# Kernel optimization log

Hardware: AMD Instinct MI355X
Metric: run time of the kernel (lower is better)

Reference implementation:

```python
import jax, jax.numpy as jnp
import numpy as np

K = 10
A_JAC = 0.5
B_JAC = 0.5
N_NODES = 100000
N_EDGES = 1600000
IN_CH, HID, OUT_CH = 256, 64, 32
NUM_LAYERS = 2


def setup_inputs() -> dict:
    key = jax.random.key(0)
    k1, k2, k3, k4, k5, k6 = jax.random.split(key, 6)
    x = jax.random.normal(k1, (N_NODES, IN_CH), dtype=jnp.float32)
    edge_index = jax.random.randint(k2, (2, N_EDGES), 0, N_NODES, dtype=jnp.int64)
    W1 = jax.random.normal(k3, (IN_CH, HID), dtype=jnp.float32) / np.sqrt(IN_CH)
    b1 = jnp.zeros((HID,), dtype=jnp.float32)
    coeffs = jnp.ones((NUM_LAYERS, K + 1), dtype=jnp.float32) / (K + 1)
    W2 = jax.random.normal(k4, (HID, OUT_CH), dtype=jnp.float32) / np.sqrt(HID)
    b2 = jnp.zeros((OUT_CH,), dtype=jnp.float32)
    return {"x": x, "edge_index": edge_index, "W1": W1, "b1": b1,
            "coeffs": coeffs, "W2": W2, "b2": b2}


def _build_norm(edge_index, num_nodes):
    # add self loops (as PyG add_self_loops does)
    loops = jnp.arange(num_nodes, dtype=edge_index.dtype)
    row = jnp.concatenate([edge_index[0], loops])
    col = jnp.concatenate([edge_index[1], loops])
    deg = jax.ops.segment_sum(jnp.ones_like(col, dtype=jnp.float32), col,
                              num_segments=num_nodes)
    dinv = jnp.where(deg > 0, deg ** -0.5, 0.0)
    norm = dinv[row] * dinv[col]  # [E + N]
    return row, col, norm


def _propagate(h, row, col, norm, num_nodes):
    # out[i] = sum_{e: col[e]=i} norm[e] * h[row[e]]
    return jax.ops.segment_sum(norm[:, None] * h[row], col, num_segments=num_nodes)


def _jacobi_conv(h, row, col, norm, c, num_nodes):
    a, b = A_JAC, B_JAC
    Tx0 = h
    out = c[0] * Tx0
    Tx1 = _propagate(h, row, col, norm, num_nodes)
    out = out + c[1] * Tx1
    for k in range(2, K + 1):
        n = k - 1
        A_n = (2 * n + a + b + 1) * (2 * n + a + b + 2) / (2 * (n + 1) * (n + a + b + 1))
        B_n = (a ** 2 - b ** 2) * (2 * n + a + b + 1) / (2 * (n + 1) * (n + a + b + 1) * (2 * n + a + b))
        C_n = (n + a) * (n + b) * (2 * n + a + b + 2) / ((n + 1) * (n + a + b + 1) * (2 * n + a + b))
        Tx2 = A_n * _propagate(Tx1, row, col, norm, num_nodes) + B_n * Tx1 - C_n * Tx0
        out = out + c[k] * Tx2
        Tx0, Tx1 = Tx1, Tx2
    return out


def reference(x, edge_index, W1, b1, coeffs, W2, b2):
    num_nodes = x.shape[0]
    row, col, norm = _build_norm(edge_index, num_nodes)
    h = jax.nn.relu(x @ W1 + b1)
    for l in range(NUM_LAYERS):
        h = jax.nn.relu(_jacobi_conv(h, row, col, norm, coeffs[l], num_nodes))
    return h @ W2 + b2
```

## Files before the change

### kernel.cpp

```cpp
#include <hip/hip_runtime.h>
#include <hip/hip_fp16.h>

#define NN 100000
#define NE 1600000
#define KORD 10
#define HID 64
#define SCAN_BLK 1024
#define NBLK ((NN + SCAN_BLK - 1) / SCAN_BLK)

typedef _Float16 half8v __attribute__((ext_vector_type(8)));
typedef _Float16 half4v __attribute__((ext_vector_type(4)));
typedef float float4v __attribute__((ext_vector_type(4)));

__device__ __forceinline__ float2 up2(unsigned u) {
    __half2 hh = *(__half2*)&u;
    return __half22float2(hh);
}
__device__ __forceinline__ unsigned pk2(float a, float b) {
    __half2 hh = __floats2half2_rn(a, b);
    return *(unsigned*)&hh;
}

__global__ __launch_bounds__(256) void k_zero(int* __restrict__ cnt,
                                              int* __restrict__ dhist) {
    int i = blockIdx.x * 256 + threadIdx.x;
    if (i < NN) cnt[i] = 0;
    if (i < 64) dhist[i] = 0;
}

__global__ __launch_bounds__(256) void k_hist(const int* __restrict__ ei,
                                              int* __restrict__ cnt) {
    int e = blockIdx.x * 256 + threadIdx.x;
    if (e < NE) atomicAdd(&cnt[ei[NE + e]], 1);
}

__global__ __launch_bounds__(256) void k_dinv(const int* __restrict__ cnt,
                                              float* __restrict__ dinv) {
    int i = blockIdx.x * 256 + threadIdx.x;
    if (i < NN) dinv[i] = rsqrtf((float)(cnt[i] + 1));
}

__global__ __launch_bounds__(SCAN_BLK) void k_scan1(const int* __restrict__ cnt,
                                                    int* __restrict__ cursor,
                                                    int* __restrict__ bsum) {
    __shared__ int tmp[SCAN_BLK];
    int t = threadIdx.x;
    int g = blockIdx.x * SCAN_BLK + t;
    int v = (g < NN) ? cnt[g] : 0;
    tmp[t] = v;
    __syncthreads();
    int x = v;
    for (int off = 1; off < SCAN_BLK; off <<= 1) {
        int y = (t >= off) ? tmp[t - off] : 0;
        __syncthreads();
        x += y;
        tmp[t] = x;
        __syncthreads();
    }
    if (g < NN) cursor[g] = x - v;
    if (t == SCAN_BLK - 1) bsum[blockIdx.x] = x;
}

__global__ __launch_bounds__(128) void k_scan2(int* __restrict__ bsum) {
    __shared__ int tmp[128];
    int t = threadIdx.x;
    int v = (t < NBLK) ? bsum[t] : 0;
    tmp[t] = v;
    __syncthreads();
    int x = v;
    for (int off = 1; off < 128; off <<= 1) {
        int y = (t >= off) ? tmp[t - off] : 0;
        __syncthreads();
        x += y;
        tmp[t] = x;
        __syncthreads();
    }
    if (t < NBLK) bsum[t] = x - v;
}

__global__ __launch_bounds__(SCAN_BLK) void k_scan3(int* __restrict__ cursor,
                                                    const int* __restrict__ bsum,
                                                    int* __restrict__ ccur) {
    int g = blockIdx.x * SCAN_BLK + threadIdx.x;
    if (g < NN) {
        int v = cursor[g] + bsum[blockIdx.x];
        cursor[g] = v;
        ccur[g] = v;
    }
    if (g == 0) cursor[NN] = NE;
}

__global__ __launch_bounds__(256) void k_scatter(const int* __restrict__ ei,
                                                 int* __restrict__ ccur,
                                                 int* __restrict__ csr) {
    int e = blockIdx.x * 256 + threadIdx.x;
    if (e >= NE) return;
    int r = ei[e], c = ei[NE + e];
    int pos = atomicAdd(&ccur[c], 1);
    csr[pos] = r;
}

__global__ __launch_bounds__(256) void k_dhist(const int* __restrict__ cnt,
                                               int* __restrict__ dhist) {
    __shared__ int lh[64];
    int t = threadIdx.x;
    if (t < 64) lh[t] = 0;
    __syncthreads();
    int i = blockIdx.x * 256 + t;
    if (i < NN) atomicAdd(&lh[min(cnt[i], 63)], 1);
    __syncthreads();
    if (t < 64 && lh[t]) atomicAdd(&dhist[t], lh[t]);
}

__global__ void k_dscan(int* __restrict__ dhist) {
    __shared__ int tmp[64];
    int t = threadIdx.x;
    int v = dhist[t];
    tmp[t] = v;
    __syncthreads();
    int x = v;
    for (int off = 1; off < 64; off <<= 1) {
        int y = (t >= off) ? tmp[t - off] : 0;
        __syncthreads();
        x += y;
        tmp[t] = x;
        __syncthreads();
    }
    dhist[t] = x - v;
}

__global__ __launch_bounds__(256) void k_dperm(const int* __restrict__ cnt,
                                               int* __restrict__ dhist,
                                               int* __restrict__ perm) {
    __shared__ int lh[64], lb[64];
    int t = threadIdx.x;
    if (t < 64) lh[t] = 0;
    __syncthreads();
    int i = blockIdx.x * 256 + t;
    int b = 0, my = 0;
    if (i < NN) { b = min(cnt[i], 63); my = atomicAdd(&lh[b], 1); }
    __syncthreads();
    if (t < 64) lb[t] = lh[t] ? atomicAdd(&dhist[t], lh[t]) : 0;
    __syncthreads();
    if (i < NN) perm[lb[b] + my] = i;
}

__global__ __launch_bounds__(256) void k_zrow(__half* __restrict__ a, __half* __restrict__ b,
                                              __half* __restrict__ c, __half* __restrict__ d) {
    int t = threadIdx.x;
    __half z = __float2half(0.f);
    size_t base = (size_t)NN * HID;
    if (t < 64)       a[base + t] = z;
    else if (t < 128) b[base + (t - 64)] = z;
    else if (t < 192) c[base + (t - 128)] = z;
    else              d[base + (t - 192)] = z;
}

__global__ __launch_bounds__(256) void k_prepw1(const float* __restrict__ W1,
                                                _Float16* __restrict__ W1T) {
    int f = blockIdx.x * 256 + threadIdx.x;
    int n = f >> 8, k = f & 255;
    W1T[f] = (_Float16)W1[k * 64 + n];
}

#define G1K 128
#define G1S 136
__global__ __launch_bounds__(256) void k_gemm1(const float* __restrict__ x,
                                               const _Float16* __restrict__ W1T,
                                               const float* __restrict__ b1,
                                               const float* __restrict__ dinv,
                                               __half* __restrict__ h) {
    __shared__ _Float16 A_lds[64 * G1S];
    __shared__ _Float16 B_lds[64 * G1S];
    int t = threadIdx.x;
    int wave = t >> 6, lane = t & 63;
    int quad = lane >> 4, m16 = lane & 15;
    int row0 = blockIdx.x * 64;

    float4v acc[4];
#pragma unroll
    for (int n4 = 0; n4 < 4; ++n4) acc[n4] = (float4v){0.f, 0.f, 0.f, 0.f};

    for (int c = 0; c < 2; ++c) {
        int k0 = c * G1K;
#pragma unroll
        for (int i = 0; i < 8; ++i) {
            int f = i * 256 + t;
            int r = f >> 5, c4 = f & 31;
            int grow = row0 + r;
            float4 v = (grow < NN) ? *(const float4*)&x[(size_t)grow * 256 + k0 + c4 * 4]
                                   : make_float4(0.f, 0.f, 0.f, 0.f);
            half4v hv = {(_Float16)v.x, (_Float16)v.y, (_Float16)v.z, (_Float16)v.w};
            *(half4v*)&A_lds[r * G1S + c4 * 4] = hv;
        }
#pragma unroll
        for (int i = 0; i < 4; ++i) {
            int f = i * 256 + t;
            int n = f >> 4, k8 = f & 15;
            *(half8v*)&B_lds[n * G1S + k8 * 8] =
                *(const half8v*)&W1T[n * 256 + k0 + k8 * 8];
        }
        __syncthreads();

#pragma unroll
        for (int s = 0; s < 4; ++s) {
            half8v af = *(const half8v*)&A_lds[(wave * 16 + m16) * G1S + s * 32 + quad * 8];
#pragma unroll
            for (int n4 = 0; n4 < 4; ++n4) {
                half8v bf = *(const half8v*)&B_lds[(n4 * 16 + m16) * G1S + s * 32 + quad * 8];
                acc[n4] = __builtin_amdgcn_mfma_f32_16x16x32_f16(af, bf, acc[n4], 0, 0, 0);
            }
        }
        __syncthreads();
    }

    float bv[4];
#pragma unroll
    for (int n4 = 0; n4 < 4; ++n4) bv[n4] = b1[n4 * 16 + m16];
#pragma unroll
    for (int r = 0; r < 4; ++r) {
        int grow = row0 + wave * 16 + quad * 4 + r;
        if (grow >= NN) continue;
        float dv = dinv[grow];
#pragma unroll
        for (int n4 = 0; n4 < 4; ++n4) {
            float v = dv * fmaxf(acc[n4][r] + bv[n4], 0.f);
            h[(size_t)grow * 64 + n4 * 16 + m16] = __float2half(v);
        }
    }
}

__global__ __launch_bounds__(256) void k_prop(const int* __restrict__ cursor,
                                              const int* __restrict__ csr,
                                              const int* __restrict__ perm,
                                              const __half* __restrict__ src,
                                              const __half* __restrict__ t0,
                                              const float* __restrict__ dinv,
                                              __half* __restrict__ dst,
                                              __half* __restrict__ acc,
                                              __half* __restrict__ hout,
                                              float An, float Bn, float Cn,
                                              const float* __restrict__ coeffs,
                                              int cbase, int kidx, int init,
                                              int finalize, int unscale) {
    int slot = ((blockIdx.x * 256 + threadIdx.x) >> 6) * 8 + ((threadIdx.x & 63) >> 3);
    int ch8 = (threadIdx.x & 7) * 8;
    bool valid = slot < NN;
    int node = valid ? perm[slot] : 0;
    int beg = valid ? cursor[node] : 0;
    int end = valid ? cursor[node + 1] : 0;

    int len = end - beg;
    int q = len >> 2;
    int j0 = beg,          e0 = beg + q;
    int j1 = e0,           e1 = beg + 2 * q;
    int j2 = e1,           e2 = beg + 3 * q;
    int j3 = e2,           e3 = end;

    float p[8];
#pragma unroll
    for (int i = 0; i < 8; ++i) p[i] = 0.f;

    while (__any(j3 < e3)) {
        int a0 = (j0 < e0) ? j0 : 0;
        int a1 = (j1 < e1) ? j1 : 0;
        int a2 = (j2 < e2) ? j2 : 0;
        int a3 = (j3 < e3) ? j3 : 0;
        int v0 = csr[a0], v1 = csr[a1], v2 = csr[a2], v3 = csr[a3];
        int r0 = (j0 < e0) ? v0 : NN;
        int r1 = (j1 < e1) ? v1 : NN;
        int r2 = (j2 < e2) ? v2 : NN;
        int r3 = (j3 < e3) ? v3 : NN;
        uint4 u0 = *(const uint4*)&src[(size_t)r0 * HID + ch8];
        uint4 u1 = *(const uint4*)&src[(size_t)r1 * HID + ch8];
        uint4 u2 = *(const uint4*)&src[(size_t)r2 * HID + ch8];
        uint4 u3 = *(const uint4*)&src[(size_t)r3 * HID + ch8];
        {
            float2 f0 = up2(u0.x), f1 = up2(u0.y), f2 = up2(u0.z), f3 = up2(u0.w);
            p[0] += f0.x; p[1] += f0.y; p[2] += f1.x; p[3] += f1.y;
            p[4] += f2.x; p[5] += f2.y; p[6] += f3.x; p[7] += f3.y;
        }
        {
            float2 f0 = up2(u1.x), f1 = up2(u1.y), f2 = up2(u1.z), f3 = up2(u1.w);
            p[0] += f0.x; p[1] += f0.y; p[2] += f1.x; p[3] += f1.y;
            p[4] += f2.x; p[5] += f2.y; p[6] += f3.x; p[7] += f3.y;
        }
        {
            float2 f0 = up2(u2.x), f1 = up2(u2.y), f2 = up2(u2.z), f3 = up2(u2.w);
            p[0] += f0.x; p[1] += f0.y; p[2] += f1.x; p[3] += f1.y;
            p[4] += f2.x; p[5] += f2.y; p[6] += f3.x; p[7] += f3.y;
        }
        {
            float2 f0 = up2(u3.x), f1 = up2(u3.y), f2 = up2(u3.z), f3 = up2(u3.w);
            p[0] += f0.x; p[1] += f0.y; p[2] += f1.x; p[3] += f1.y;
            p[4] += f2.x; p[5] += f2.y; p[6] += f3.x; p[7] += f3.y;
        }
        ++j0; ++j1; ++j2; ++j3;
    }

    if (!valid) return;
    size_t idx = (size_t)node * HID + ch8;
    float dv = dinv[node];
    float dv2 = dv * dv;

    uint4 sr = *(const uint4*)&src[idx];
    float2 s01 = up2(sr.x), s23 = up2(sr.y), s45 = up2(sr.z), s67 = up2(sr.w);
    float sv[8] = {s01.x, s01.y, s23.x, s23.y, s45.x, s45.y, s67.x, s67.y};

    uint4 tr = *(const uint4*)&t0[idx];
    float2 t01 = up2(tr.x), t23 = up2(tr.y), t45 = up2(tr.z), t67 = up2(tr.w);
    float tv[8] = {t01.x, t01.y, t23.x, t23.y, t45.x, t45.y, t67.x, t67.y};

    float v[8];
#pragma unroll
    for (int i = 0; i < 8; ++i)
        v[i] = An * dv2 * (p[i] + sv[i]) + Bn * sv[i] - Cn * tv[i];

    if (!finalize) {
        uint4 o;
        o.x = pk2(v[0], v[1]); o.y = pk2(v[2], v[3]);
        o.z = pk2(v[4], v[5]); o.w = pk2(v[6], v[7]);
        *(uint4*)&dst[idx] = o;
    }

    float ck = coeffs[cbase + kidx];
    float av[8];
    if (init) {
        float c0 = coeffs[cbase];
#pragma unroll
        for (int i = 0; i < 8; ++i) av[i] = c0 * sv[i];
    } else {
        uint4 ar = *(const uint4*)&acc[idx];
        float2 a01 = up2(ar.x), a23 = up2(ar.y), a45 = up2(ar.z), a67 = up2(ar.w);
        av[0] = a01.x; av[1] = a01.y; av[2] = a23.x; av[3] = a23.y;
        av[4] = a45.x; av[5] = a45.y; av[6] = a67.x; av[7] = a67.y;
    }
#pragma unroll
    for (int i = 0; i < 8; ++i) av[i] += ck * v[i];

    uint4 o;
    if (finalize) {
        float s = unscale ? (1.0f / dv) : 1.0f;
        o.x = pk2(s * fmaxf(av[0], 0.f), s * fmaxf(av[1], 0.f));
        o.y = pk2(s * fmaxf(av[2], 0.f), s * fmaxf(av[3], 0.f));
        o.z = pk2(s * fmaxf(av[4], 0.f), s * fmaxf(av[5], 0.f));
        o.w = pk2(s * fmaxf(av[6], 0.f), s * fmaxf(av[7], 0.f));
        *(uint4*)&hout[idx] = o;
    } else {
        o.x = pk2(av[0], av[1]); o.y = pk2(av[2], av[3]);
        o.z = pk2(av[4], av[5]); o.w = pk2(av[6], av[7]);
        *(uint4*)&acc[idx] = o;
    }
}

__global__ __launch_bounds__(256) void k_gemm2(const __half* __restrict__ h,
                                               const float* __restrict__ W2,
                                               const float* __restrict__ b2,
                                               float* __restrict__ out) {
    __shared__ float W2s[64 * 32];
    __shared__ float b2s[32];
    int t = threadIdx.x;
    for (int i = t * 4; i < 64 * 32; i += 256 * 4)
        *(float4*)&W2s[i] = *(const float4*)&W2[i];
    if (t < 32) b2s[t] = b2[t];
    __syncthreads();

    int gid = blockIdx.x * 256 + t;
    int row = gid >> 3;
    int c4 = (t & 7) * 4;
    if (row >= NN) return;
    const __half* hr = h + (size_t)row * 64;
    float4 acc = *(const float4*)&b2s[c4];
#pragma unroll
    for (int k8 = 0; k8 < 8; ++k8) {
        uint4 raw = *(const uint4*)&hr[k8 * 8];
        float2 a01 = up2(raw.x), a23 = up2(raw.y), a45 = up2(raw.z), a67 = up2(raw.w);
        float a[8] = {a01.x, a01.y, a23.x, a23.y, a45.x, a45.y, a67.x, a67.y};
#pragma unroll
        for (int j = 0; j < 8; ++j) {
            float4 w = *(const float4*)&W2s[(k8 * 8 + j) * 32 + c4];
            acc.x += a[j] * w.x;
            acc.y += a[j] * w.y;
            acc.z += a[j] * w.z;
            acc.w += a[j] * w.w;
        }
    }
    *(float4*)&out[(size_t)row * 32 + c4] = acc;
}

extern "C" void kernel_launch(void* const* d_in, const int* in_sizes, int n_in,
                              void* d_out, int out_size, void* d_ws, size_t ws_size,
                              hipStream_t stream) {
    const float* x      = (const float*)d_in[0];
    const int*   ei     = (const int*)d_in[1];
    const float* W1     = (const float*)d_in[2];
    const float* b1     = (const float*)d_in[3];
    const float* coeffs = (const float*)d_in[4];
    const float* W2     = (const float*)d_in[5];
    const float* b2     = (const float*)d_in[6];
    float* out = (float*)d_out;

    char* ws = (char*)d_ws;
    size_t off = 0;
    auto alloc = [&](size_t bytes) { void* p = ws + off; off += (bytes + 255) & ~(size_t)255; return p; };
    int*      cnt    = (int*)alloc(NN * 4);
    int*      cursor = (int*)alloc((NN + 1) * 4);
    int*      ccur   = (int*)alloc(NN * 4);
    int*      bsum   = (int*)alloc(NBLK * 4);
    float*    dinv   = (float*)alloc(NN * 4);
    int*      csr    = (int*)alloc((size_t)NE * 4);
    int*      dhist  = (int*)alloc(64 * 4);
    int*      perm   = (int*)alloc(NN * 4);
    _Float16* W1T    = (_Float16*)alloc(256 * 64 * 2);
    __half*   h16    = (__half*)alloc((size_t)(NN + 1) * HID * 2);
    __half*   bufA   = (__half*)alloc((size_t)(NN + 1) * HID * 2);
    __half*   bufB   = (__half*)alloc((size_t)(NN + 1) * HID * 2);
    __half*   bufC   = (__half*)alloc((size_t)(NN + 1) * HID * 2);
    __half*   accb   = (__half*)alloc((size_t)NN * HID * 2);

    const int BN = (NN + 255) / 256;
    const int BE = (NE + 255) / 256;
    const int BP = (NN + 31) / 32;

    k_zero<<<BN, 256, 0, stream>>>(cnt, dhist);
    k_hist<<<BE, 256, 0, stream>>>(ei, cnt);
    k_dinv<<<BN, 256, 0, stream>>>(cnt, dinv);
    k_scan1<<<NBLK, SCAN_BLK, 0, stream>>>(cnt, cursor, bsum);
    k_scan2<<<1, 128, 0, stream>>>(bsum);
    k_scan3<<<NBLK, SCAN_BLK, 0, stream>>>(cursor, bsum, ccur);
    k_scatter<<<BE, 256, 0, stream>>>(ei, ccur, csr);

    k_dhist<<<BN, 256, 0, stream>>>(cnt, dhist);
    k_dscan<<<1, 64, 0, stream>>>(dhist);
    k_dperm<<<BN, 256, 0, stream>>>(cnt, dhist, perm);
    k_zrow<<<1, 256, 0, stream>>>(h16, bufA, bufB, bufC);

    k_prepw1<<<64, 256, 0, stream>>>(W1, W1T);
    k_gemm1<<<(NN + 63) / 64, 256, 0, stream>>>(x, W1T, b1, dinv, h16);

    __half* rot[4] = {h16, bufA, bufB, bufC};

    for (int l = 0; l < 2; ++l) {
        int cbase = l * (KORD + 1);
        k_prop<<<BP, 256, 0, stream>>>(cursor, csr, perm, rot[0], rot[0], dinv,
                                       rot[1], accb, h16, 1.0f, 0.0f, 0.0f,
                                       coeffs, cbase, 1, 1, 0, 0);
        for (int k = 2; k <= KORD; ++k) {
            __half* dst = rot[k & 3];
            const __half* s1 = rot[(k - 1) & 3];
            const __half* s0 = rot[(k - 2) & 3];
            double n = k - 1, a = 0.5, b = 0.5;
            double An = (2*n + a + b + 1) * (2*n + a + b + 2) / (2 * (n + 1) * (n + a + b + 1));
            double Bn = (a*a - b*b) * (2*n + a + b + 1) / (2 * (n + 1) * (n + a + b + 1) * (2*n + a + b));
            double Cn = (n + a) * (n + b) * (2*n + a + b + 2) / ((n + 1) * (n + a + b + 1) * (2*n + a + b));
            k_prop<<<BP, 256, 0, stream>>>(cursor, csr, perm, s1, s0, dinv,
                                           dst, accb, h16, (float)An, (float)Bn, (float)Cn,
                                           coeffs, cbase, k, 0,
                                           (k == KORD) ? 1 : 0, l);
        }
    }

    k_gemm2<<<(NN * 8 + 255) / 256, 256, 0, stream>>>(h16, W2, b2, out);
}
```

Before: 1.173 ms.

## Build CSR with two-pass bucketed binning instead of global atomic scatter

Replaces the histogram, three-kernel scan and atomic scatter CSR build with a two-level bucket sort. The first pass bins edges into 256-node buckets using shared-memory atomics and packs the local column and source row into one word. The second pass sorts each bucket in LDS and also writes the degree, dinv and cursor. This cuts global atomics and kernel launches, but adds a fixed per-bucket capacity (BCAP) that silently drops edges if a bucket overflows, and assumes the row index fits in 24 bits.

```diff
diff --git a/kernel.cpp b/kernel.cpp
--- a/kernel.cpp
+++ b/kernel.cpp
@@ -5,8 +5,10 @@
 #define NE 1600000
 #define KORD 10
 #define HID 64
-#define SCAN_BLK 1024
-#define NBLK ((NN + SCAN_BLK - 1) / SCAN_BLK)
+
+#define NBUK ((NN + 255) / 256)
+#define BCAP 8192
+#define EPB  (NE / 256)
 
 typedef _Float16 half8v __attribute__((ext_vector_type(8)));
 typedef _Float16 half4v __attribute__((ext_vector_type(4)));
@@ -21,83 +23,104 @@
     return *(unsigned*)&hh;
 }
 
-__global__ __launch_bounds__(256) void k_zero(int* __restrict__ cnt,
+__global__ __launch_bounds__(512) void k_zero(int* __restrict__ gcnt,
                                               int* __restrict__ dhist) {
-    int i = blockIdx.x * 256 + threadIdx.x;
-    if (i < NN) cnt[i] = 0;
-    if (i < 64) dhist[i] = 0;
-}
-
-__global__ __launch_bounds__(256) void k_hist(const int* __restrict__ ei,
-                                              int* __restrict__ cnt) {
-    int e = blockIdx.x * 256 + threadIdx.x;
-    if (e < NE) atomicAdd(&cnt[ei[NE + e]], 1);
-}
-
-__global__ __launch_bounds__(256) void k_dinv(const int* __restrict__ cnt,
-                                              float* __restrict__ dinv) {
-    int i = blockIdx.x * 256 + threadIdx.x;
-    if (i < NN) dinv[i] = rsqrtf((float)(cnt[i] + 1));
-}
-
-__global__ __launch_bounds__(SCAN_BLK) void k_scan1(const int* __restrict__ cnt,
-                                                    int* __restrict__ cursor,
-                                                    int* __restrict__ bsum) {
-    __shared__ int tmp[SCAN_BLK];
-    int t = threadIdx.x;
-    int g = blockIdx.x * SCAN_BLK + t;
-    int v = (g < NN) ? cnt[g] : 0;
+    int t = threadIdx.x;
+    if (t < NBUK) gcnt[t] = 0;
+    if (t < 64) dhist[t] = 0;
+}
+
+__global__ __launch_bounds__(1024) void k_binA(const int* __restrict__ ei,
+                                               int* __restrict__ gcnt,
+                                               unsigned* __restrict__ staged) {
+    __shared__ int lh[NBUK];
+    __shared__ int lcur[NBUK];
+    int t = threadIdx.x;
+    int ebeg = blockIdx.x * EPB;
+    int eend = min(ebeg + EPB, NE);
+    for (int i = t; i < NBUK; i += 1024) lh[i] = 0;
+    __syncthreads();
+    for (int e = ebeg + t; e < eend; e += 1024)
+        atomicAdd(&lh[ei[NE + e] >> 8], 1);
+    __syncthreads();
+    for (int i = t; i < NBUK; i += 1024)
+        lcur[i] = lh[i] ? atomicAdd(&gcnt[i], lh[i]) : 0;
+    __syncthreads();
+    for (int e = ebeg + t; e < eend; e += 1024) {
+        int r = ei[e], c = ei[NE + e];
+        int bkt = c >> 8;
+        int slot = atomicAdd(&lcur[bkt], 1);
+        if (slot < BCAP)
+            staged[(size_t)bkt * BCAP + slot] = ((unsigned)(c & 255) << 24) | (unsigned)r;
+    }
+}
+
+__global__ __launch_bounds__(512) void k_bscan(const int* __restrict__ gcnt,
+                                               int* __restrict__ bbase,
+                                               int* __restrict__ cursor) {
+    __shared__ int tmp[512];
+    int t = threadIdx.x;
+    int v = (t < NBUK) ? gcnt[t] : 0;
     tmp[t] = v;
     __syncthreads();
     int x = v;
-    for (int off = 1; off < SCAN_BLK; off <<= 1) {
+    for (int off = 1; off < 512; off <<= 1) {
         int y = (t >= off) ? tmp[t - off] : 0;
         __syncthreads();
         x += y;
         tmp[t] = x;
         __syncthreads();
     }
-    if (g < NN) cursor[g] = x - v;
-    if (t == SCAN_BLK - 1) bsum[blockIdx.x] = x;
-}
-
-__global__ __launch_bounds__(128) void k_scan2(int* __restrict__ bsum) {
-    __shared__ int tmp[128];
-    int t = threadIdx.x;
-    int v = (t < NBLK) ? bsum[t] : 0;
-    tmp[t] = v;
-    __syncthreads();
-    int x = v;
-    for (int off = 1; off < 128; off <<= 1) {
-        int y = (t >= off) ? tmp[t - off] : 0;
-        __syncthreads();
-        x += y;
-        tmp[t] = x;
-        __syncthreads();
-    }
-    if (t < NBLK) bsum[t] = x - v;
-}
-
-__global__ __launch_bounds__(SCAN_BLK) void k_scan3(int* __restrict__ cursor,
-                                                    const int* __restrict__ bsum,
-                                                    int* __restrict__ ccur) {
-    int g = blockIdx.x * SCAN_BLK + threadIdx.x;
-    if (g < NN) {
-        int v = cursor[g] + bsum[blockIdx.x];
-        cursor[g] = v;
-        ccur[g] = v;
-    }
-    if (g == 0) cursor[NN] = NE;
-}
-
-__global__ __launch_bounds__(256) void k_scatter(const int* __restrict__ ei,
-                                                 int* __restrict__ ccur,
-                                                 int* __restrict__ csr) {
-    int e = blockIdx.x * 256 + threadIdx.x;
-    if (e >= NE) return;
-    int r = ei[e], c = ei[NE + e];
-    int pos = atomicAdd(&ccur[c], 1);
-    csr[pos] = r;
+    if (t < NBUK) bbase[t] = x - v;
+    if (t == 0) cursor[NN] = NE;
+}
+
+__global__ __launch_bounds__(512) void k_binB(const unsigned* __restrict__ staged,
+                                              const int* __restrict__ gcnt,
+                                              const int* __restrict__ bbase,
+                                              int* __restrict__ cursor,
+                                              int* __restrict__ cnt,
+                                              float* __restrict__ dinv,
+                                              int* __restrict__ csr) {
+    __shared__ unsigned lrec[BCAP];
+    __shared__ int lcnt[256], lcur[256], ltmp[256];
+    int b = blockIdx.x, t = threadIdx.x;
+    int count = min(gcnt[b], BCAP);
+    int base = bbase[b];
+    if (t < 256) lcnt[t] = 0;
+    __syncthreads();
+    for (int i = t; i < count; i += 512) {
+        unsigned rec = staged[(size_t)b * BCAP + i];
+        lrec[i] = rec;
+        atomicAdd(&lcnt[rec >> 24], 1);
+    }
+    __syncthreads();
+    int v = 0, x = 0;
+    if (t < 256) { v = lcnt[t]; ltmp[t] = v; }
+    __syncthreads();
+    x = v;
+    for (int off = 1; off < 256; off <<= 1) {
+        int y = (t < 256 && t >= off) ? ltmp[t - off] : 0;
+        __syncthreads();
+        if (t < 256) { x += y; ltmp[t] = x; }
+        __syncthreads();
+    }
+    if (t < 256) {
+        int excl = x - v;
+        lcur[t] = base + excl;
+        int node = b * 256 + t;
+        if (node < NN) {
+            cursor[node] = base + excl;
+            cnt[node] = v;
+            dinv[node] = rsqrtf((float)(v + 1));
+        }
+    }
+    __syncthreads();
+    for (int i = t; i < count; i += 512) {
+        unsigned rec = lrec[i];
+        int pos = atomicAdd(&lcur[rec >> 24], 1);
+        csr[pos] = (int)(rec & 0xFFFFFFu);
+    }
 }
 
 __global__ __launch_bounds__(256) void k_dhist(const int* __restrict__ cnt,
@@ -405,12 +428,13 @@
     auto alloc = [&](size_t bytes) { void* p = ws + off; off += (bytes + 255) & ~(size_t)255; return p; };
     int*      cnt    = (int*)alloc(NN * 4);
     int*      cursor = (int*)alloc((NN + 1) * 4);
-    int*      ccur   = (int*)alloc(NN * 4);
-    int*      bsum   = (int*)alloc(NBLK * 4);
     float*    dinv   = (float*)alloc(NN * 4);
     int*      csr    = (int*)alloc((size_t)NE * 4);
     int*      dhist  = (int*)alloc(64 * 4);
     int*      perm   = (int*)alloc(NN * 4);
+    int*      gcnt   = (int*)alloc(NBUK * 4);
+    int*      bbase  = (int*)alloc(NBUK * 4);
+    unsigned* staged = (unsigned*)alloc((size_t)NBUK * BCAP * 4);
     _Float16* W1T    = (_Float16*)alloc(256 * 64 * 2);
     __half*   h16    = (__half*)alloc((size_t)(NN + 1) * HID * 2);
     __half*   bufA   = (__half*)alloc((size_t)(NN + 1) * HID * 2);
@@ -419,16 +443,12 @@
     __half*   accb   = (__half*)alloc((size_t)NN * HID * 2);
 
     const int BN = (NN + 255) / 256;
-    const int BE = (NE + 255) / 256;
     const int BP = (NN + 31) / 32;
 
-    k_zero<<<BN, 256, 0, stream>>>(cnt, dhist);
-    k_hist<<<BE, 256, 0, stream>>>(ei, cnt);
-    k_dinv<<<BN, 256, 0, stream>>>(cnt, dinv);
-    k_scan1<<<NBLK, SCAN_BLK, 0, stream>>>(cnt, cursor, bsum);
-    k_scan2<<<1, 128, 0, stream>>>(bsum);
-    k_scan3<<<NBLK, SCAN_BLK, 0, stream>>>(cursor, bsum, ccur);
-    k_scatter<<<BE, 256, 0, stream>>>(ei, ccur, csr);
+    k_zero<<<1, 512, 0, stream>>>(gcnt, dhist);
+    k_binA<<<256, 1024, 0, stream>>>(ei, gcnt, staged);
+    k_bscan<<<1, 512, 0, stream>>>(gcnt, bbase, cursor);
+    k_binB<<<NBUK, 512, 0, stream>>>(staged, gcnt, bbase, cursor, cnt, dinv, csr);
 
     k_dhist<<<BN, 256, 0, stream>>>(cnt, dhist);
     k_dscan<<<1, 64, 0, stream>>>(dhist);
```

Result: faster. 1.040 ms (-11.3%).
